# Kernel tuning notes

Hardware: AMD Instinct MI355X
Metric: run time of the kernel (lower is better)

## Reference

```python
import jax, jax.numpy as jnp
import numpy as np

V, D, NL, NH, HD, FF = 32000, 216, 11, 4, 54, 864
B, S = 2, 1024
EPS = 1e-5
THETA = 10000.0


def setup_inputs() -> dict:
    key = jax.random.key(0)
    ks = jax.random.split(key, 8)
    sc = 0.02
    return {
        "input_ids": jax.random.randint(ks[0], (B, S), 0, V),
        "embed": jax.random.normal(ks[1], (V, D), jnp.float32) * sc,
        "ln1_w": jnp.ones((NL, D), jnp.float32),
        "qkv_w": jax.random.normal(ks[2], (NL, 3 * D, D), jnp.float32) * sc,
        "o_w": jax.random.normal(ks[3], (NL, D, D), jnp.float32) * sc,
        "ln2_w": jnp.ones((NL, D), jnp.float32),
        "gate_w": jax.random.normal(ks[4], (NL, FF, D), jnp.float32) * sc,
        "up_w": jax.random.normal(ks[5], (NL, FF, D), jnp.float32) * sc,
        "down_w": jax.random.normal(ks[6], (NL, D, FF), jnp.float32) * sc,
        "norm_w": jnp.ones((D,), jnp.float32),
        "lm_head_w": jax.random.normal(ks[7], (V, D), jnp.float32) * sc,
    }


def _rmsnorm(x, w):
    return x * jax.lax.rsqrt(jnp.mean(x * x, axis=-1, keepdims=True) + EPS) * w


def _rope_tables(seq_len, dim, dtype):
    inv_freq = 1.0 / (THETA ** (jnp.arange(0, dim, 2, dtype=jnp.float32) / dim))
    t = jnp.arange(seq_len, dtype=jnp.float32)
    freqs = jnp.outer(t, inv_freq)              # [S, dim/2]
    emb = jnp.concatenate([freqs, freqs], -1)   # [S, dim]
    return jnp.cos(emb).astype(dtype), jnp.sin(emb).astype(dtype)


def _rotate_half(x):
    x1, x2 = x[..., : x.shape[-1] // 2], x[..., x.shape[-1] // 2:]
    return jnp.concatenate([-x2, x1], axis=-1)


def _forward(input_ids, embed, ln1_w, qkv_w, o_w, ln2_w, gate_w, up_w, down_w, norm_w, lm_head_w):
    b, s = input_ids.shape
    x = embed[input_ids]                                       # [B,S,D]
    cos, sin = _rope_tables(s, HD, x.dtype)                    # [S,HD]
    scale = HD ** -0.5
    neg_inf = jnp.finfo(x.dtype).min
    causal = jnp.triu(jnp.ones((s, s), bool), k=1)             # [S,S]

    for i in range(NL):
        # self-attention
        h = _rmsnorm(x, ln1_w[i])
        qkv = jnp.einsum("bsd,ed->bse", h, qkv_w[i])           # [B,S,3D]
        qkv = qkv.reshape(b, s, 3, NH, HD).transpose(2, 0, 3, 1, 4)  # [3,B,H,S,HD]
        q, k, v = qkv[0], qkv[1], qkv[2]
        q = q * cos + _rotate_half(q) * sin
        k = k * cos + _rotate_half(k) * sin
        scores = jnp.einsum("bhqd,bhkd->bhqk", q, k) * scale
        scores = jnp.where(causal, neg_inf, scores)
        attn = jax.nn.softmax(scores, axis=-1)
        out = jnp.einsum("bhqk,bhkd->bhqd", attn, v)
        out = out.transpose(0, 2, 1, 3).reshape(b, s, D)
        x = x + jnp.einsum("bsd,ed->bse", out, o_w[i])
        # SwiGLU MLP
        h = _rmsnorm(x, ln2_w[i])
        gate = jnp.einsum("bsd,fd->bsf", h, gate_w[i])
        up = jnp.einsum("bsd,fd->bsf", h, up_w[i])
        x = x + jnp.einsum("bsf,df->bsd", jax.nn.silu(gate) * up, down_w[i])

    x = _rmsnorm(x, norm_w)
    logits = jnp.einsum("bsd,vd->bsv", x, lm_head_w)           # [B,S,V]
    return logits


def reference(input_ids, embed, ln1_w, qkv_w, o_w, ln2_w, gate_w, up_w, down_w, norm_w, lm_head_w):
    return _forward(input_ids, embed, ln1_w, qkv_w, o_w, ln2_w, gate_w, up_w, down_w, norm_w, lm_head_w)
```

## Files before the change

### kernel.cpp

```cpp
#include <hip/hip_runtime.h>
#include <math.h>

#define Vv 32000
#define Dm 216
#define NLAY 11
#define NHh 4
#define HDd 54
#define FFf 864
#define Bb 2
#define Ss 1024
#define Tt (Bb*Ss)
#define EPSf 1e-5f
#define QKVW 648
#define KP 224
#define HDP 64
#define VTSZ (Ss*HDP)

typedef __attribute__((ext_vector_type(8))) short short8;
typedef __attribute__((ext_vector_type(8))) unsigned short ushort8;
typedef __attribute__((ext_vector_type(4))) float f32x4;

__device__ __forceinline__ unsigned short f2bf(float f) {
    unsigned int u = __float_as_uint(f);
    return (unsigned short)((u + 0x7fffu + ((u >> 16) & 1u)) >> 16);
}
__device__ __forceinline__ float bf2f(unsigned short u) {
    return __uint_as_float(((unsigned int)u) << 16);
}

__device__ void dev_convw(int relb, int nblk, const float* __restrict__ src,
                          unsigned short* __restrict__ dst,
                          int L, int N, int K, int Npad, int Kp, int rstride,
                          long dls, long doff) {
    size_t total = (size_t)L * Npad * Kp;
    for (size_t idx = (size_t)relb * 256 + threadIdx.x; idx < total;
         idx += (size_t)nblk * 256) {
        int k = (int)(idx % Kp);
        size_t rr = idx / Kp;
        int n = (int)(rr % Npad);
        int l = (int)(rr / Npad);
        float v = (n < N && k < K) ? src[((size_t)l * N + n) * K + k] : 0.f;
        dst[(size_t)l * dls + doff + (size_t)n * rstride + k] = f2bf(v);
    }
}

__device__ void dev_convqkv(int relb, int nblk, const float* __restrict__ src,
                            unsigned short* __restrict__ dst) {
    size_t total = (size_t)NLAY * 768 * KP;
    for (size_t idx = (size_t)relb * 256 + threadIdx.x; idx < total;
         idx += (size_t)nblk * 256) {
        int kk2 = (int)(idx % KP);
        size_t rr = idx / KP;
        int nr = (int)(rr % 768);
        int l = (int)(rr / 768);
        float v = 0.f;
        if (nr < 648 && kk2 < 216) {
            int srow;
            float sc = 1.f;
            if (nr < 432) {
                int which = nr >= 216;
                int cih = nr - which * 216;
                int head = cih / 54, dd = cih % 54;
                int j = dd >> 1, odd = dd & 1;
                srow = which * 216 + head * 54 + j + odd * 27;
                if (!which) sc = 0.13608276348795434f;
            } else srow = nr;
            v = src[((size_t)l * QKVW + srow) * 216 + kk2] * sc;
        }
        dst[idx] = f2bf(v);
    }
}

__device__ void dev_convowh(int relb, int nblk, const float* __restrict__ src,
                            unsigned short* __restrict__ dst) {
    size_t total = (size_t)NLAY * 4 * 224 * 64;
    for (size_t idx = (size_t)relb * 256 + threadIdx.x; idx < total;
         idx += (size_t)nblk * 256) {
        int kk = (int)(idx & 63);
        size_t rr = idx >> 6;
        int n = (int)(rr % 224);
        size_t rh = rr / 224;
        int h = (int)(rh & 3);
        int l = (int)(rh >> 2);
        float v = (n < 216 && kk < 54)
            ? src[((size_t)l * 216 + n) * 216 + h * 54 + kk] : 0.f;
        dst[idx] = f2bf(v);
    }
}

__global__ void k_setup(const int* __restrict__ ids, const float* __restrict__ emb,
                        float* __restrict__ x,
                        float* __restrict__ cost, float* __restrict__ sint,
                        unsigned int* __restrict__ zp, size_t zwords,
                        const float* __restrict__ qkv_w, unsigned short* __restrict__ qkvw,
                        const float* __restrict__ o_w, unsigned short* __restrict__ owh,
                        const float* __restrict__ gate_w, const float* __restrict__ up_w,
                        unsigned short* __restrict__ guw,
                        const float* __restrict__ down_w, unsigned short* __restrict__ dww,
                        const float* __restrict__ lm_w, unsigned short* __restrict__ lmw)
{
    const int b = blockIdx.x;
    const int tid = threadIdx.x;
    if (b < 2048) {
        int id = ids[b];
        for (int d = tid; d < Dm; d += 256)
            x[(size_t)b * Dm + d] = emb[(size_t)id * Dm + d];
    } else if (b < 2176) {
        for (int idx = (b - 2048) * 256 + tid; idx < 1024 * 27; idx += 128 * 256) {
            int s = idx / 27, j = idx % 27;
            float inv = powf(10000.0f, -2.0f * (float)j / 54.0f);
            float f = (float)s * inv;
            cost[s * 27 + j] = cosf(f);
            sint[s * 27 + j] = sinf(f);
        }
    } else if (b < 2432) {
        for (size_t i = (size_t)(b - 2176) * 256 + tid; i < zwords; i += (size_t)256 * 256)
            zp[i] = 0;
    } else if (b < 2944) {
        dev_convqkv(b - 2432, 512, qkv_w, qkvw);
    } else if (b < 3200) {
        dev_convowh(b - 2944, 256, o_w, owh);
    } else if (b < 3712) {
        dev_convw(b - 3200, 512, gate_w, guw, NLAY, FFf, Dm, 896, KP, 2 * KP, 1792L * KP, 0);
    } else if (b < 4224) {
        dev_convw(b - 3712, 512, up_w, guw, NLAY, FFf, Dm, 896, KP, 2 * KP, 1792L * KP, KP);
    } else if (b < 4736) {
        dev_convw(b - 4224, 512, down_w, dww, NLAY, Dm, FFf, 256, 864, 864, 256L * 864, 0);
    } else {
        dev_convw(b - 4736, 1024, lm_w, lmw, 1, Vv, Dm, Vv, KP, KP, (long)Vv * KP, 0);
    }
}

__device__ __forceinline__ void normpro(const float* __restrict__ x,
                                        const float* __restrict__ lnw, int m0,
                                        float* rsl, float* lnl, int tid) {
    __syncthreads();
    if (tid < 224) lnl[tid] = (tid < 216) ? lnw[tid] : 0.f;
    if (tid < 128) {
        int row = tid >> 1, half = tid & 1;
        const float* xr = x + (size_t)(m0 + row) * Dm + half * 108;
        float ss = 0.f;
        #pragma unroll
        for (int q = 0; q < 27; ++q) {
            float4 v = *(const float4*)(xr + q * 4);
            ss += v.x * v.x + v.y * v.y + v.z * v.z + v.w * v.w;
        }
        ss += __shfl_xor(ss, 1, 64);
        if (half == 0) rsl[row] = rsqrtf(ss / 216.f + EPSf);
    }
    __syncthreads();
}

__device__ __forceinline__ ushort8 normA(const float* __restrict__ x,
                                         const float* rsl, const float* lnl,
                                         int m0, int row, int base) {
    ushort8 o;
    if (base < 216) {
        const float* pp = x + (size_t)(m0 + row) * Dm + base;
        float r = rsl[row];
        float4 v0 = *(const float4*)pp;
        float4 v1 = *(const float4*)(pp + 4);
        o[0] = f2bf(v0.x * r * lnl[base + 0]);
        o[1] = f2bf(v0.y * r * lnl[base + 1]);
        o[2] = f2bf(v0.z * r * lnl[base + 2]);
        o[3] = f2bf(v0.w * r * lnl[base + 3]);
        o[4] = f2bf(v1.x * r * lnl[base + 4]);
        o[5] = f2bf(v1.y * r * lnl[base + 5]);
        o[6] = f2bf(v1.z * r * lnl[base + 6]);
        o[7] = f2bf(v1.w * r * lnl[base + 7]);
    } else {
        #pragma unroll
        for (int e = 0; e < 8; ++e) o[e] = 0;
    }
    return o;
}

__global__ __launch_bounds__(256) void k_qkv64(
    const float* __restrict__ x, const unsigned short* __restrict__ W,
    const float* __restrict__ lnw,
    const float* __restrict__ cost, const float* __restrict__ sint,
    unsigned short* __restrict__ Qb, unsigned short* __restrict__ Kb,
    unsigned short* __restrict__ Vt)
{
    __shared__ __align__(16) unsigned char SM[17664];
    unsigned short* lA = (unsigned short*)SM;
    unsigned short* lB = (unsigned short*)(SM + 8192);
    float* rsl = (float*)(SM + 16384);
    float* lnl = (float*)(SM + 16640);
    const int tid = threadIdx.x;
    const int m0 = blockIdx.x * 64;
    const int n0 = blockIdx.y * 64;
    normpro(x, lnw, m0, rsl, lnl, tid);

    const int wid = tid >> 6, lane = tid & 63;
    const int wr = wid >> 1, wc = wid & 1;
    const int r = tid >> 2, kc = tid & 3;
    const int lo = (r >> 4) * 512 + (((kc << 4) | (r & 15)) << 3);

    ushort8 ra = normA(x, rsl, lnl, m0, r, kc * 8);
    ushort8 rb = *(const ushort8*)(W + (size_t)(n0 + r) * KP + kc * 8);
    *(ushort8*)&lA[lo] = ra;
    *(ushort8*)&lB[lo] = rb;
    __syncthreads();

    f32x4 acc[2][2] = {};
    int cur = 0;
    for (int step = 0; step < 7; ++step) {
        const bool more = step < 6;
        if (more) {
            const int k0 = (step + 1) << 5;
            ra = normA(x, rsl, lnl, m0, r, k0 + kc * 8);
            rb = *(const ushort8*)(W + (size_t)(n0 + r) * KP + k0 + kc * 8);
        }
        short8 af[2], bf2[2];
        #pragma unroll
        for (int f = 0; f < 2; ++f) {
            af[f] = *(const short8*)&lA[cur * 2048 + (wr * 2 + f) * 512 + lane * 8];
            bf2[f] = *(const short8*)&lB[cur * 2048 + (wc * 2 + f) * 512 + lane * 8];
        }
        #pragma unroll
        for (int fm = 0; fm < 2; ++fm)
            #pragma unroll
            for (int fn = 0; fn < 2; ++fn)
                acc[fm][fn] = __builtin_amdgcn_mfma_f32_16x16x32_bf16(af[fm], bf2[fn], acc[fm][fn], 0, 0, 0);
        if (more) {
            const int nxt = cur ^ 1;
            *(ushort8*)&lA[nxt * 2048 + lo] = ra;
            *(ushort8*)&lB[nxt * 2048 + lo] = rb;
            __syncthreads();
            cur = nxt;
        }
    }

    const int lc16 = lane & 15, lg = lane >> 4;
    #pragma unroll
    for (int fm = 0; fm < 2; ++fm) {
        const int mrow = m0 + wr * 32 + fm * 16 + lg * 4;
        const int b = mrow >> 10;
        const int st0 = mrow & 1023;
        #pragma unroll
        for (int fn = 0; fn < 2; ++fn) {
            const int ncol = n0 + wc * 32 + fn * 16 + lc16;
            float v0 = acc[fm][fn][0], v1 = acc[fm][fn][1];
            float v2 = acc[fm][fn][2], v3 = acc[fm][fn][3];
            float p0 = __shfl_xor(v0, 1, 64);
            float p1 = __shfl_xor(v1, 1, 64);
            float p2 = __shfl_xor(v2, 1, 64);
            float p3 = __shfl_xor(v3, 1, 64);
            if (ncol < 432) {
                int which = ncol >= 216;
                int cih = ncol - which * 216;
                int head = cih / 54, dd = cih % 54;
                int j = dd >> 1;
                bool odd = dd & 1;
                unsigned short* dst = (which ? Kb : Qb) +
                    ((size_t)(b * NHh + head) * Ss + st0) * HDP + dd;
                float vv[4] = {v0, v1, v2, v3};
                float pp[4] = {p0, p1, p2, p3};
                #pragma unroll
                for (int i = 0; i < 4; ++i) {
                    float c = cost[(st0 + i) * 27 + j];
                    float sn = sint[(st0 + i) * 27 + j];
                    float o = odd ? (vv[i] * c + pp[i] * sn) : (vv[i] * c - pp[i] * sn);
                    dst[(size_t)i * HDP] = f2bf(o);
                }
            } else if (ncol < 648) {
                int d = ncol - 432;
                int head = d / 54, dd = d % 54;
                ushort4 pk;
                pk.x = f2bf(v0); pk.y = f2bf(v1); pk.z = f2bf(v2); pk.w = f2bf(v3);
                *(ushort4*)(Vt + (size_t)(b * NHh + head) * VTSZ + (size_t)dd * Ss + st0) = pk;
            }
        }
    }
}

__global__ __launch_bounds__(256) void k_gateup64(
    const float* __restrict__ x, const unsigned short* __restrict__ W,
    const float* __restrict__ lnw, unsigned short* __restrict__ act)
{
    __shared__ __align__(16) unsigned char SM[17664];
    unsigned short* lA = (unsigned short*)SM;
    unsigned short* lB = (unsigned short*)(SM + 8192);
    float* rsl = (float*)(SM + 16384);
    float* lnl = (float*)(SM + 16640);
    const int tid = threadIdx.x;
    const int m0 = blockIdx.x * 64;
    const int n0 = blockIdx.y * 64;
    normpro(x, lnw, m0, rsl, lnl, tid);

    const int wid = tid >> 6, lane = tid & 63;
    const int wr = wid >> 1, wc = wid & 1;
    const int r = tid >> 2, kc = tid & 3;
    const int lo = (r >> 4) * 512 + (((kc << 4) | (r & 15)) << 3);

    ushort8 ra = normA(x, rsl, lnl, m0, r, kc * 8);
    ushort8 rb = *(const ushort8*)(W + (size_t)(n0 + r) * KP + kc * 8);
    *(ushort8*)&lA[lo] = ra;
    *(ushort8*)&lB[lo] = rb;
    __syncthreads();

    f32x4 acc[2][2] = {};
    int cur = 0;
    for (int step = 0; step < 7; ++step) {
        const bool more = step < 6;
        if (more) {
            const int k0 = (step + 1) << 5;
            ra = normA(x, rsl, lnl, m0, r, k0 + kc * 8);
            rb = *(const ushort8*)(W + (size_t)(n0 + r) * KP + k0 + kc * 8);
        }
        short8 af[2], bf2[2];
        #pragma unroll
        for (int f = 0; f < 2; ++f) {
            af[f] = *(const short8*)&lA[cur * 2048 + (wr * 2 + f) * 512 + lane * 8];
            bf2[f] = *(const short8*)&lB[cur * 2048 + (wc * 2 + f) * 512 + lane * 8];
        }
        #pragma unroll
        for (int fm = 0; fm < 2; ++fm)
            #pragma unroll
            for (int fn = 0; fn < 2; ++fn)
                acc[fm][fn] = __builtin_amdgcn_mfma_f32_16x16x32_bf16(af[fm], bf2[fn], acc[fm][fn], 0, 0, 0);
        if (more) {
            const int nxt = cur ^ 1;
            *(ushort8*)&lA[nxt * 2048 + lo] = ra;
            *(ushort8*)&lB[nxt * 2048 + lo] = rb;
            __syncthreads();
            cur = nxt;
        }
    }

    const int lc16 = lane & 15, lg = lane >> 4;
    #pragma unroll
    for (int fm = 0; fm < 2; ++fm) {
        const int mrow = m0 + wr * 32 + fm * 16 + lg * 4;
        #pragma unroll
        for (int fn = 0; fn < 2; ++fn) {
            const int ncol = n0 + wc * 32 + fn * 16 + lc16;
            #pragma unroll
            for (int i = 0; i < 4; ++i) {
                float v = acc[fm][fn][i];
                float p = __shfl_xor(v, 1, 64);
                if ((lc16 & 1) == 0 && ncol < 1728) {
                    float y = v / (1.f + __expf(-v)) * p;
                    act[(size_t)(mrow + i) * 864 + (ncol >> 1)] = f2bf(y);
                }
            }
        }
    }
}

__global__ __launch_bounds__(256) void k_gemm_s(
    const unsigned short* __restrict__ A, const unsigned short* __restrict__ W,
    float* __restrict__ xio, int N, int Kp)
{
    __shared__ __align__(16) unsigned short lA[2][2048];
    __shared__ __align__(16) unsigned short lB[2][2048];
    const int tid = threadIdx.x;
    const int m0 = blockIdx.x * 64, n0 = blockIdx.y * 64;
    const int wid = tid >> 6, lane = tid & 63;
    const int wr = wid >> 1, wc = wid & 1;
    const int nsteps = Kp >> 5;
    const int r = tid >> 2, kc = tid & 3;
    const int lo = (r >> 4) * 512 + (((kc << 4) | (r & 15)) << 3);

    ushort8 ra = *(const ushort8*)(A + (size_t)(m0 + r) * Kp + kc * 8);
    ushort8 rb = *(const ushort8*)(W + (size_t)(n0 + r) * Kp + kc * 8);
    *(ushort8*)&lA[0][lo] = ra;
    *(ushort8*)&lB[0][lo] = rb;
    __syncthreads();

    f32x4 acc[2][2] = {};
    int cur = 0;
    for (int step = 0; step < nsteps; ++step) {
        const bool more = (step + 1) < nsteps;
        if (more) {
            const int k0 = (step + 1) << 5;
            ra = *(const ushort8*)(A + (size_t)(m0 + r) * Kp + k0 + kc * 8);
            rb = *(const ushort8*)(W + (size_t)(n0 + r) * Kp + k0 + kc * 8);
        }
        short8 af[2], bf2[2];
        #pragma unroll
        for (int f = 0; f < 2; ++f) {
            af[f] = *(const short8*)&lA[cur][(wr * 2 + f) * 512 + lane * 8];
            bf2[f] = *(const short8*)&lB[cur][(wc * 2 + f) * 512 + lane * 8];
        }
        #pragma unroll
        for (int fm = 0; fm < 2; ++fm)
            #pragma unroll
            for (int fn = 0; fn < 2; ++fn)
                acc[fm][fn] = __builtin_amdgcn_mfma_f32_16x16x32_bf16(af[fm], bf2[fn], acc[fm][fn], 0, 0, 0);
        if (more) {
            const int nxt = cur ^ 1;
            *(ushort8*)&lA[nxt][lo] = ra;
            *(ushort8*)&lB[nxt][lo] = rb;
            __syncthreads();
            cur = nxt;
        }
    }

    #pragma unroll
    for (int fm = 0; fm < 2; ++fm) {
        const int mrow = m0 + wr * 32 + fm * 16 + (lane >> 4) * 4;
        #pragma unroll
        for (int fn = 0; fn < 2; ++fn) {
            const int ncol = n0 + wc * 32 + fn * 16 + (lane & 15);
            if (ncol < N) {
                #pragma unroll
                for (int i = 0; i < 4; ++i) {
                    const size_t oi = (size_t)(mrow + i) * N + ncol;
                    xio[oi] += acc[fm][fn][i];
                }
            }
        }
    }
}

__global__ __launch_bounds__(256) void k_attn_o16(
    const unsigned short* __restrict__ Qb, const unsigned short* __restrict__ Kb,
    const unsigned short* __restrict__ Vt, const unsigned short* __restrict__ owh_l,
    float* __restrict__ x)
{
    __shared__ __align__(16) unsigned char SM[38912];
    const int tid = threadIdx.x;
    const int qu = blockIdx.x, h = blockIdx.y, b = blockIdx.z;
    const int bh = b * NHh + h;
    const int q0w = qu * 16;
    const int w = tid >> 6, lane = tid & 63;
    const int lc = lane & 15, lg = lane >> 4;

    unsigned short* Klw = (unsigned short*)(SM + w * 4096);
    unsigned short* Vlw = (unsigned short*)(SM + 16384 + w * 4096);
    unsigned short* Plw = (unsigned short*)(SM + 32768 + w * 1024);
    unsigned short* Ol  = (unsigned short*)(SM + 36864);

    const unsigned short* Qp = Qb + (size_t)bh * VTSZ;
    const unsigned short* Kpp = Kb + (size_t)bh * VTSZ;
    const unsigned short* Vp = Vt + (size_t)bh * VTSZ;
    const unsigned short* owh_h = owh_l + (size_t)h * 224 * 64;

    short8 qa[2];
    #pragma unroll
    for (int half = 0; half < 2; ++half)
        qa[half] = *(const short8*)(Qp + (size_t)(q0w + lc) * HDP + lg * 8 + half * 32);

    f32x4 o4[4] = {};
    float mreg[4] = {-3e38f, -3e38f, -3e38f, -3e38f};
    float lreg[4] = {0.f, 0.f, 0.f, 0.f};

    const int nt = (q0w + 15) / 32 + 1;
    for (int t = w; t < nt; t += 4) {
        const int kv0 = t * 32;
        for (int c = lane; c < 512; c += 64) {
            if (c < 256) {
                int sub = c >> 6;
                int kgrp = sub >> 1, dhalf = sub & 1;
                int dchunk = (c >> 4) & 3, krow = c & 15;
                *(ushort8*)&Klw[sub * 512 + (c & 63) * 8] =
                    *(const ushort8*)(Kpp + (size_t)(kv0 + kgrp * 16 + krow) * HDP + dhalf * 32 + dchunk * 8);
            } else {
                int c2 = c - 256;
                int dgrp = c2 >> 6;
                int kchunk = (c2 >> 4) & 3, dcol = c2 & 15;
                *(ushort8*)&Vlw[dgrp * 512 + (c2 & 63) * 8] =
                    *(const ushort8*)(Vp + (size_t)(dgrp * 16 + dcol) * Ss + kv0 + kchunk * 8);
            }
        }
        f32x4 s4[2] = {};
        #pragma unroll
        for (int dhalf = 0; dhalf < 2; ++dhalf) {
            #pragma unroll
            for (int kgrp = 0; kgrp < 2; ++kgrp) {
                short8 kf = *(const short8*)&Klw[(kgrp * 2 + dhalf) * 512 + lane * 8];
                s4[kgrp] = __builtin_amdgcn_mfma_f32_16x16x32_bf16(qa[dhalf], kf, s4[kgrp], 0, 0, 0);
            }
        }
        if (kv0 + 31 > q0w) {
            #pragma unroll
            for (int kgrp = 0; kgrp < 2; ++kgrp) {
                int kg = kv0 + kgrp * 16 + lc;
                #pragma unroll
                for (int rr = 0; rr < 4; ++rr) {
                    int qg = q0w + lg * 4 + rr;
                    if (kg > qg) s4[kgrp][rr] = -3e38f;
                }
            }
        }
        #pragma unroll
        for (int rr = 0; rr < 4; ++rr) {
            float rm = fmaxf(s4[0][rr], s4[1][rr]);
            #pragma unroll
            for (int msk = 1; msk < 16; msk <<= 1)
                rm = fmaxf(rm, __shfl_xor(rm, msk, 64));
            float mn = fmaxf(mreg[rr], rm);
            float esc = __expf(mreg[rr] - mn);
            mreg[rr] = mn;
            float e0 = __expf(s4[0][rr] - mn);
            float e1 = __expf(s4[1][rr] - mn);
            float rs = e0 + e1;
            #pragma unroll
            for (int msk = 1; msk < 16; msk <<= 1)
                rs += __shfl_xor(rs, msk, 64);
            lreg[rr] = lreg[rr] * esc + rs;
            #pragma unroll
            for (int db = 0; db < 4; ++db) o4[db][rr] *= esc;
            int q = lg * 4 + rr;
            Plw[(((lc >> 3)) * 16 + q) * 8 + (lc & 7)] = f2bf(e0);
            Plw[((2 + (lc >> 3)) * 16 + q) * 8 + (lc & 7)] = f2bf(e1);
        }
        short8 pa = *(const short8*)&Plw[(lg * 16 + lc) * 8];
        #pragma unroll
        for (int db = 0; db < 4; ++db) {
            short8 vf = *(const short8*)&Vlw[db * 512 + lane * 8];
            o4[db] = __builtin_amdgcn_mfma_f32_16x16x32_bf16(pa, vf, o4[db], 0, 0, 0);
        }
    }

    __syncthreads();
    float* mg = (float*)SM;
    const int slot = (w * 64 + lane) * 25;
    #pragma unroll
    for (int rr = 0; rr < 4; ++rr) { mg[slot + rr] = mreg[rr]; mg[slot + 4 + rr] = lreg[rr]; }
    #pragma unroll
    for (int db = 0; db < 4; ++db)
        #pragma unroll
        for (int rr = 0; rr < 4; ++rr) mg[slot + 8 + db * 4 + rr] = o4[db][rr];
    __syncthreads();
    if (w == 0) {
        #pragma unroll
        for (int rr = 0; rr < 4; ++rr) {
            float m = mreg[rr];
            #pragma unroll
            for (int ww = 1; ww < 4; ++ww)
                m = fmaxf(m, mg[(ww * 64 + lane) * 25 + rr]);
            float eself = __expf(mreg[rr] - m);
            float l = lreg[rr] * eself;
            float oc[4];
            #pragma unroll
            for (int db = 0; db < 4; ++db) oc[db] = o4[db][rr] * eself;
            #pragma unroll
            for (int ww = 1; ww < 4; ++ww) {
                int sl = (ww * 64 + lane) * 25;
                float e = __expf(mg[sl + rr] - m);
                l += mg[sl + 4 + rr] * e;
                #pragma unroll
                for (int db = 0; db < 4; ++db) oc[db] += mg[sl + 8 + db * 4 + rr] * e;
            }
            float inv = 1.f / l;
            int q = lg * 4 + rr;
            #pragma unroll
            for (int db = 0; db < 4; ++db) {
                int kchunk = db * 2 + (lc >> 3);
                Ol[(kchunk * 16 + q) * 8 + (lc & 7)] = f2bf(oc[db] * inv);
            }
        }
    }
    __syncthreads();

    f32x4 oacc[4] = {};
    #pragma unroll
    for (int ks = 0; ks < 2; ++ks) {
        short8 afr = *(const short8*)&Ol[ks * 512 + lane * 8];
        #pragma unroll
        for (int gi = 0; gi < 4; ++gi) {
            int g = gi * 4 + w;
            if (g < 14) {
                int n = g * 16 + lc;
                short8 bfr = *(const short8*)(owh_h + (size_t)n * 64 + ks * 32 + lg * 8);
                oacc[gi] = __builtin_amdgcn_mfma_f32_16x16x32_bf16(afr, bfr, oacc[gi], 0, 0, 0);
            }
        }
    }
    #pragma unroll
    for (int gi = 0; gi < 4; ++gi) {
        int g = gi * 4 + w;
        if (g < 14) {
            int col = g * 16 + lc;
            if (col < 216) {
                #pragma unroll
                for (int i = 0; i < 4; ++i) {
                    int row = b * Ss + q0w + lg * 4 + i;
                    atomicAdd(&x[(size_t)row * Dm + col], oacc[gi][i]);
                }
            }
        }
    }
}

template<int OUTM, bool NORMA>
__global__ __launch_bounds__(256, 2) void k_gemm_f(
    const void* __restrict__ Av, const unsigned short* __restrict__ W,
    const float* __restrict__ res, void* __restrict__ outv,
    const float* __restrict__ lnw, int N, int Kp)
{
    __shared__ __align__(16) unsigned short lds[2][2][4096];
    __shared__ float rsl[128];
    __shared__ float lnl[224];
    const int tid = threadIdx.x;
    const int m0 = blockIdx.x * 128;
    const int n0 = blockIdx.y * 128;
    const int wid = tid >> 6, lane = tid & 63;
    const int wr = wid >> 1, wc = wid & 1;
    const int nsteps = Kp >> 5;

    if constexpr (NORMA) {
        const float* Af = (const float*)Av;
        if (tid < 224) lnl[tid] = (tid < 216) ? lnw[tid] : 0.f;
        int row = tid >> 1, half = tid & 1;
        const float* xr = Af + (size_t)(m0 + row) * 216 + half * 108;
        float ss = 0.f;
        #pragma unroll
        for (int q = 0; q < 27; ++q) {
            float4 v = *(const float4*)(xr + q * 4);
            ss += v.x * v.x + v.y * v.y + v.z * v.z + v.w * v.w;
        }
        ss += __shfl_xor(ss, 1, 64);
        if (half == 0) rsl[row] = rsqrtf(ss / 216.f + EPSf);
        __syncthreads();
    }

    const int i0 = tid, i1 = tid + 256;
    const int rA0 = i0 >> 2, cA0 = i0 & 3;
    const int rA1 = i1 >> 2, cA1 = i1 & 3;
    const int lo0 = (rA0 >> 4) * 512 + (((cA0 << 4) | (rA0 & 15)) << 3);
    const int lo1 = (rA1 >> 4) * 512 + (((cA1 << 4) | (rA1 & 15)) << 3);

    auto loadA = [&](int row, int base) -> ushort8 {
        ushort8 o;
        if constexpr (NORMA) {
            if (base < 216) {
                const float* p = (const float*)Av + (size_t)(m0 + row) * 216 + base;
                float r = rsl[row];
                float4 v0 = *(const float4*)p;
                float4 v1 = *(const float4*)(p + 4);
                o[0] = f2bf(v0.x * r * lnl[base + 0]);
                o[1] = f2bf(v0.y * r * lnl[base + 1]);
                o[2] = f2bf(v0.z * r * lnl[base + 2]);
                o[3] = f2bf(v0.w * r * lnl[base + 3]);
                o[4] = f2bf(v1.x * r * lnl[base + 4]);
                o[5] = f2bf(v1.y * r * lnl[base + 5]);
                o[6] = f2bf(v1.z * r * lnl[base + 6]);
                o[7] = f2bf(v1.w * r * lnl[base + 7]);
            } else {
                #pragma unroll
                for (int e = 0; e < 8; ++e) o[e] = 0;
            }
        } else {
            o = *(const ushort8*)((const unsigned short*)Av + (size_t)(m0 + row) * Kp + base);
        }
        return o;
    };

    ushort8 ra0, ra1, rb0, rb1;
    ra0 = loadA(rA0, cA0 * 8);
    ra1 = loadA(rA1, cA1 * 8);
    rb0 = *(const ushort8*)(W + (size_t)(n0 + rA0) * Kp + cA0 * 8);
    rb1 = *(const ushort8*)(W + (size_t)(n0 + rA1) * Kp + cA1 * 8);
    *(ushort8*)&lds[0][0][lo0] = ra0;
    *(ushort8*)&lds[0][0][lo1] = ra1;
    *(ushort8*)&lds[0][1][lo0] = rb0;
    *(ushort8*)&lds[0][1][lo1] = rb1;
    __syncthreads();

    f32x4 acc[4][4] = {};
    int cur = 0;
    for (int step = 0; step < nsteps; ++step) {
        const bool more = (step + 1) < nsteps;
        if (more) {
            const int k0 = (step + 1) << 5;
            ra0 = loadA(rA0, k0 + cA0 * 8);
            ra1 = loadA(rA1, k0 + cA1 * 8);
            rb0 = *(const ushort8*)(W + (size_t)(n0 + rA0) * Kp + k0 + cA0 * 8);
            rb1 = *(const ushort8*)(W + (size_t)(n0 + rA1) * Kp + k0 + cA1 * 8);
        }
        short8 af[4], bf[4];
        #pragma unroll
        for (int f = 0; f < 4; ++f) {
            af[f] = *(const short8*)&lds[cur][0][(wr * 4 + f) * 512 + lane * 8];
            bf[f] = *(const short8*)&lds[cur][1][(wc * 4 + f) * 512 + lane * 8];
        }
        #pragma unroll
        for (int fm = 0; fm < 4; ++fm)
            #pragma unroll
            for (int fn = 0; fn < 4; ++fn)
                acc[fm][fn] = __builtin_amdgcn_mfma_f32_16x16x32_bf16(af[fm], bf[fn], acc[fm][fn], 0, 0, 0);
        if (more) {
            const int nxt = cur ^ 1;
            *(ushort8*)&lds[nxt][0][lo0] = ra0;
            *(ushort8*)&lds[nxt][0][lo1] = ra1;
            *(ushort8*)&lds[nxt][1][lo0] = rb0;
            *(ushort8*)&lds[nxt][1][lo1] = rb1;
            __syncthreads();
            cur = nxt;
        }
    }

    const int lc16 = lane & 15;
    #pragma unroll
    for (int fm = 0; fm < 4; ++fm) {
        const int mrow = m0 + wr * 64 + fm * 16 + (lane >> 4) * 4;
        #pragma unroll
        for (int fn = 0; fn < 4; ++fn) {
            const int ncol = n0 + wc * 64 + fn * 16 + lc16;
            if (ncol < N) {
                #pragma unroll
                for (int i = 0; i < 4; ++i) {
                    const size_t oi = (size_t)(mrow + i) * N + ncol;
                    float v = acc[fm][fn][i];
                    if (res) v += res[oi];
                    ((float*)outv)[oi] = v;
                }
            }
        }
    }
}

__global__ void k_embed(const int* __restrict__ ids, const float* __restrict__ emb,
                        float* __restrict__ x) {
    int t = blockIdx.x;
    int id = ids[t];
    for (int d = threadIdx.x; d < Dm; d += blockDim.x)
        x[(size_t)t * Dm + d] = emb[(size_t)id * Dm + d];
}

__global__ void k_rope_tables(float* __restrict__ cosb, float* __restrict__ sinb) {
    int s = blockIdx.x;
    for (int d = threadIdx.x; d < HDd; d += blockDim.x) {
        int j = d % (HDd / 2);
        float inv = powf(10000.0f, -2.0f * (float)j / (float)HDd);
        float f = (float)s * inv;
        cosb[s * HDd + d] = cosf(f);
        sinb[s * HDd + d] = sinf(f);
    }
}

__global__ void k_rmsnorm(const float* __restrict__ x, const float* __restrict__ w,
                          float* __restrict__ h) {
    int t = blockIdx.x;
    const float* xr = x + (size_t)t * Dm;
    float ss = 0.f;
    for (int d = threadIdx.x; d < Dm; d += 64) { float v = xr[d]; ss += v * v; }
    for (int o = 32; o; o >>= 1) ss += __shfl_down(ss, o, 64);
    float r = __shfl(ss, 0, 64);
    r = rsqrtf(r / (float)Dm + EPSf);
    for (int d = threadIdx.x; d < Dm; d += 64)
        h[(size_t)t * Dm + d] = xr[d] * r * w[d];
}

#define TS 16
__global__ void k_gemm(const float* __restrict__ A, const float* __restrict__ W,
                       const float* __restrict__ res, float* __restrict__ out,
                       int M, int N, int K) {
    __shared__ float As[TS][TS + 1];
    __shared__ float Wsm[TS][TS + 1];
    const int tx = threadIdx.x, ty = threadIdx.y;
    const int m = blockIdx.y * TS + ty;
    const int n = blockIdx.x * TS + tx;
    float acc = 0.f;
    for (int k0 = 0; k0 < K; k0 += TS) {
        int ka = k0 + tx;
        As[ty][tx] = (m < M && ka < K) ? A[(size_t)m * K + ka] : 0.f;
        int nw = blockIdx.x * TS + ty;
        Wsm[ty][tx] = (nw < N && ka < K) ? W[(size_t)nw * K + ka] : 0.f;
        __syncthreads();
        #pragma unroll
        for (int kk = 0; kk < TS; ++kk) acc += As[ty][kk] * Wsm[tx][kk];
        __syncthreads();
    }
    if (m < M && n < N) {
        float r = res ? res[(size_t)m * N + n] : 0.f;
        out[(size_t)m * N + n] = r + acc;
    }
}

__global__ void k_gateup(const float* __restrict__ A, const float* __restrict__ Wg,
                         const float* __restrict__ Wu, float* __restrict__ act,
                         int M, int N, int K) {
    __shared__ float As[TS][TS + 1];
    __shared__ float Gs[TS][TS + 1];
    __shared__ float Us[TS][TS + 1];
    const int tx = threadIdx.x, ty = threadIdx.y;
    const int m = blockIdx.y * TS + ty;
    const int n = blockIdx.x * TS + tx;
    float ag = 0.f, au = 0.f;
    for (int k0 = 0; k0 < K; k0 += TS) {
        int ka = k0 + tx;
        As[ty][tx] = (m < M && ka < K) ? A[(size_t)m * K + ka] : 0.f;
        int nw = blockIdx.x * TS + ty;
        Gs[ty][tx] = (nw < N && ka < K) ? Wg[(size_t)nw * K + ka] : 0.f;
        Us[ty][tx] = (nw < N && ka < K) ? Wu[(size_t)nw * K + ka] : 0.f;
        __syncthreads();
        #pragma unroll
        for (int kk = 0; kk < TS; ++kk) {
            ag += As[ty][kk] * Gs[tx][kk];
            au += As[ty][kk] * Us[tx][kk];
        }
        __syncthreads();
    }
    if (m < M && n < N) {
        float sg = ag / (1.f + expf(-ag));
        act[(size_t)m * N + n] = sg * au;
    }
}

__global__ void k_rope(float* __restrict__ qkv, const float* __restrict__ cosb,
                       const float* __restrict__ sinb) {
    const int t = blockIdx.x;
    const int s = t % Ss;
    float* base = qkv + (size_t)t * QKVW;
    const int HALF = HDd / 2;
    int i = threadIdx.x;
    if (i < 2 * NHh * HALF) {
        int which = i / (NHh * HALF);
        int rem = i % (NHh * HALF);
        int hh = rem / HALF;
        int d = rem % HALF;
        float* ptr = base + which * Dm + hh * HDd;
        float x1 = ptr[d], x2 = ptr[d + HALF];
        float c1 = cosb[s * HDd + d], s1 = sinb[s * HDd + d];
        float c2 = cosb[s * HDd + d + HALF], s2 = sinb[s * HDd + d + HALF];
        ptr[d]        = x1 * c1 - x2 * s1;
        ptr[d + HALF] = x2 * c2 + x1 * s2;
    }
}

__global__ void k_attn(const float* __restrict__ qkv, float* __restrict__ aout) {
    const int q = blockIdx.x, h = blockIdx.y, b = blockIdx.z;
    const int tid = threadIdx.x;
    __shared__ float p[Ss];
    __shared__ float qv[HDd];
    __shared__ float rmax[4], rsum[4];
    const size_t base = (size_t)b * Ss * QKVW;
    const float* qrow = qkv + base + (size_t)q * QKVW + h * HDd;
    if (tid < HDd) qv[tid] = qrow[tid];
    __syncthreads();
    const int nk = q + 1;
    const float scale = 0.13608276348795434f;
    float lmax = -3.0e38f;
    for (int k = tid; k < nk; k += 256) {
        const float* krow = qkv + base + (size_t)k * QKVW + Dm + h * HDd;
        float acc = 0.f;
        #pragma unroll
        for (int d = 0; d < HDd; ++d) acc += qv[d] * krow[d];
        acc *= scale;
        p[k] = acc;
        lmax = fmaxf(lmax, acc);
    }
    for (int o = 32; o; o >>= 1) lmax = fmaxf(lmax, __shfl_down(lmax, o, 64));
    if ((tid & 63) == 0) rmax[tid >> 6] = lmax;
    __syncthreads();
    const float m = fmaxf(fmaxf(rmax[0], rmax[1]), fmaxf(rmax[2], rmax[3]));
    float lsum = 0.f;
    for (int k = tid; k < nk; k += 256) {
        float e = expf(p[k] - m);
        p[k] = e;
        lsum += e;
    }
    for (int o = 32; o; o >>= 1) lsum += __shfl_down(lsum, o, 64);
    if ((tid & 63) == 0) rsum[tid >> 6] = lsum;
    __syncthreads();
    const float inv = 1.f / (rsum[0] + rsum[1] + rsum[2] + rsum[3]);
    for (int d = tid; d < HDd; d += 256) {
        const float* vcol = qkv + base + 2 * Dm + h * HDd + d;
        float acc = 0.f;
        for (int k = 0; k < nk; ++k) acc += p[k] * vcol[(size_t)k * QKVW];
        aout[(size_t)(b * Ss + q) * Dm + h * HDd + d] = acc * inv;
    }
}

extern "C" void kernel_launch(void* const* d_in, const int* in_sizes, int n_in,
                              void* d_out, int out_size, void* d_ws, size_t ws_size,
                              hipStream_t stream) {
    const int*   ids    = (const int*)d_in[0];
    const float* emb    = (const float*)d_in[1];
    const float* ln1_w  = (const float*)d_in[2];
    const float* qkv_w  = (const float*)d_in[3];
    const float* o_w    = (const float*)d_in[4];
    const float* ln2_w  = (const float*)d_in[5];
    const float* gate_w = (const float*)d_in[6];
    const float* up_w   = (const float*)d_in[7];
    const float* down_w = (const float*)d_in[8];
    const float* norm_w = (const float*)d_in[9];
    const float* lm_w   = (const float*)d_in[10];
    float* out = (float*)d_out;

    char* base = (char*)d_ws;
    size_t off = 0;
    auto carve = [&](size_t bytes) -> char* {
        char* p = base + off;
        off += (bytes + 255) & ~(size_t)255;
        return p;
    };

    float* x     = (float*)carve((size_t)Tt * Dm * 4);
    float* cos27 = (float*)carve((size_t)Ss * 27 * 4);
    float* sin27 = (float*)carve((size_t)Ss * 27 * 4);
    unsigned short* Qb   = (unsigned short*)carve((size_t)Bb * NHh * VTSZ * 2);
    unsigned short* Kb   = (unsigned short*)carve((size_t)Bb * NHh * VTSZ * 2);
    unsigned short* Vt   = (unsigned short*)carve((size_t)Bb * NHh * VTSZ * 2);
    char* zend = base + off;
    unsigned short* act  = (unsigned short*)carve((size_t)Tt * FFf * 2);
    unsigned short* qkvw = (unsigned short*)carve((size_t)NLAY * 768 * KP * 2);
    unsigned short* owh  = (unsigned short*)carve((size_t)NLAY * 4 * 224 * 64 * 2);
    unsigned short* guw  = (unsigned short*)carve((size_t)NLAY * 1792 * KP * 2);
    unsigned short* dww  = (unsigned short*)carve((size_t)NLAY * 256 * 864 * 2);
    unsigned short* lmw  = (unsigned short*)carve((size_t)Vv * KP * 2);
    size_t need = off;

    if (ws_size >= need) {
        size_t zwords = (size_t)(zend - (char*)Qb) / 4;
        k_setup<<<5760, 256, 0, stream>>>(ids, emb, x, cos27, sin27,
            (unsigned int*)Qb, zwords, qkv_w, qkvw, o_w, owh,
            gate_w, up_w, guw, down_w, dww, lm_w, lmw);

        for (int l = 0; l < NLAY; ++l) {
            k_qkv64<<<dim3(32, 12), 256, 0, stream>>>(
                x, qkvw + (size_t)l * 768 * KP, ln1_w + (size_t)l * Dm,
                cos27, sin27, Qb, Kb, Vt);
            k_attn_o16<<<dim3(64, NHh, Bb), 256, 0, stream>>>(
                Qb, Kb, Vt, owh + (size_t)l * 4 * 224 * 64, x);
            k_gateup64<<<dim3(32, 28), 256, 0, stream>>>(
                x, guw + (size_t)l * 1792 * KP, ln2_w + (size_t)l * Dm, act);
            k_gemm_s<<<dim3(32, 4), 256, 0, stream>>>(
                act, dww + (size_t)l * 256 * 864, x, Dm, 864);
        }
        k_gemm_f<0, true><<<dim3(16, 250), 256, 0, stream>>>(
            x, lmw, nullptr, out, norm_w, Vv, KP);
    } else {
        float* ws = (float*)d_ws;
        size_t o2 = 0;
        float* x2    = ws + o2; o2 += (size_t)Tt * Dm;
        float* h2    = ws + o2; o2 += (size_t)Tt * Dm;
        float* qkv2  = ws + o2; o2 += (size_t)Tt * QKVW;
        float* aout2 = ws + o2; o2 += (size_t)Tt * Dm;
        float* act2  = ws + o2; o2 += (size_t)Tt * FFf;
        float* cosb2 = ws + o2; o2 += (size_t)Ss * HDd;
        float* sinb2 = ws + o2; o2 += (size_t)Ss * HDd;

        k_embed<<<Tt, 256, 0, stream>>>(ids, emb, x2);
        k_rope_tables<<<Ss, 64, 0, stream>>>(cosb2, sinb2);
        dim3 blk(TS, TS);
        for (int l = 0; l < NLAY; ++l) {
            k_rmsnorm<<<Tt, 64, 0, stream>>>(x2, ln1_w + (size_t)l * Dm, h2);
            k_gemm<<<dim3((QKVW + TS - 1) / TS, (Tt + TS - 1) / TS), blk, 0, stream>>>(
                h2, qkv_w + (size_t)l * QKVW * Dm, nullptr, qkv2, Tt, QKVW, Dm);
            k_rope<<<Tt, 256, 0, stream>>>(qkv2, cosb2, sinb2);
            k_attn<<<dim3(Ss, NHh, Bb), 256, 0, stream>>>(qkv2, aout2);
            k_gemm<<<dim3((Dm + TS - 1) / TS, (Tt + TS - 1) / TS), blk, 0, stream>>>(
                aout2, o_w + (size_t)l * Dm * Dm, x2, x2, Tt, Dm, Dm);
            k_rmsnorm<<<Tt, 64, 0, stream>>>(x2, ln2_w + (size_t)l * Dm, h2);
            k_gateup<<<dim3((FFf + TS - 1) / TS, (Tt + TS - 1) / TS), blk, 0, stream>>>(
                h2, gate_w + (size_t)l * FFf * Dm, up_w + (size_t)l * FFf * Dm, act2, Tt, FFf, Dm);
            k_gemm<<<dim3((Dm + TS - 1) / TS, (Tt + TS - 1) / TS), blk, 0, stream>>>(
                act2, down_w + (size_t)l * Dm * FFf, x2, x2, Tt, Dm, FFf);
        }
        k_rmsnorm<<<Tt, 64, 0, stream>>>(x2, norm_w, h2);
        k_gemm<<<dim3((Vv + TS - 1) / TS, (Tt + TS - 1) / TS), blk, 0, stream>>>(
            h2, lm_w, nullptr, out, Tt, Vv, Dm);
    }
}
```

Baseline: 902.4 us.

## Fuse SwiGLU gate/up and down projection into one per-16-row FFN kernel

Replaces the separate gate/up GEMM and down-projection GEMM with a single kernel that normalizes 16 rows, computes the SwiGLU activation into shared memory, and immediately applies the down projection with a residual add. This removes the global activation buffer round-trip and one launch per layer. In exchange, only 128 blocks run and each streams the full weight matrices directly from global memory without shared-memory staging, which lowers parallelism and weight reuse.

```diff
diff --git a/kernel.cpp b/kernel.cpp
--- a/kernel.cpp
+++ b/kernel.cpp
@@ -275,140 +275,93 @@
     }
 }
 
-__global__ __launch_bounds__(256) void k_gateup64(
-    const float* __restrict__ x, const unsigned short* __restrict__ W,
-    const float* __restrict__ lnw, unsigned short* __restrict__ act)
+__global__ __launch_bounds__(256) void k_ffn16(
+    const float* __restrict__ x_in, float* __restrict__ x,
+    const unsigned short* __restrict__ guw_l, const unsigned short* __restrict__ dww_l,
+    const float* __restrict__ lnw)
 {
-    __shared__ __align__(16) unsigned char SM[17664];
-    unsigned short* lA = (unsigned short*)SM;
-    unsigned short* lB = (unsigned short*)(SM + 8192);
-    float* rsl = (float*)(SM + 16384);
-    float* lnl = (float*)(SM + 16640);
+    __shared__ __align__(16) unsigned char SM[35776];
+    unsigned short* Al  = (unsigned short*)SM;
+    unsigned short* Act = (unsigned short*)(SM + 7168);
+    float* rsl = (float*)(SM + 34816);
+    float* lnl = (float*)(SM + 34880);
     const int tid = threadIdx.x;
-    const int m0 = blockIdx.x * 64;
-    const int n0 = blockIdx.y * 64;
-    normpro(x, lnw, m0, rsl, lnl, tid);
-
-    const int wid = tid >> 6, lane = tid & 63;
-    const int wr = wid >> 1, wc = wid & 1;
-    const int r = tid >> 2, kc = tid & 3;
-    const int lo = (r >> 4) * 512 + (((kc << 4) | (r & 15)) << 3);
-
-    ushort8 ra = normA(x, rsl, lnl, m0, r, kc * 8);
-    ushort8 rb = *(const ushort8*)(W + (size_t)(n0 + r) * KP + kc * 8);
-    *(ushort8*)&lA[lo] = ra;
-    *(ushort8*)&lB[lo] = rb;
-    __syncthreads();
-
-    f32x4 acc[2][2] = {};
-    int cur = 0;
-    for (int step = 0; step < 7; ++step) {
-        const bool more = step < 6;
-        if (more) {
-            const int k0 = (step + 1) << 5;
-            ra = normA(x, rsl, lnl, m0, r, k0 + kc * 8);
-            rb = *(const ushort8*)(W + (size_t)(n0 + r) * KP + k0 + kc * 8);
-        }
-        short8 af[2], bf2[2];
-        #pragma unroll
-        for (int f = 0; f < 2; ++f) {
-            af[f] = *(const short8*)&lA[cur * 2048 + (wr * 2 + f) * 512 + lane * 8];
-            bf2[f] = *(const short8*)&lB[cur * 2048 + (wc * 2 + f) * 512 + lane * 8];
-        }
-        #pragma unroll
-        for (int fm = 0; fm < 2; ++fm)
-            #pragma unroll
-            for (int fn = 0; fn < 2; ++fn)
-                acc[fm][fn] = __builtin_amdgcn_mfma_f32_16x16x32_bf16(af[fm], bf2[fn], acc[fm][fn], 0, 0, 0);
-        if (more) {
-            const int nxt = cur ^ 1;
-            *(ushort8*)&lA[nxt * 2048 + lo] = ra;
-            *(ushort8*)&lB[nxt * 2048 + lo] = rb;
-            __syncthreads();
-            cur = nxt;
-        }
-    }
-
-    const int lc16 = lane & 15, lg = lane >> 4;
+    const int m0 = blockIdx.x * 16;
+    const int w = tid >> 6, lane = tid & 63;
+    const int lc = lane & 15, lg = lane >> 4;
+
+    if (tid < 224) lnl[tid] = (tid < 216) ? lnw[tid] : 0.f;
+    if (tid < 32) {
+        int row = tid >> 1, half = tid & 1;
+        const float* xr = x_in + (size_t)(m0 + row) * Dm + half * 108;
+        float ss = 0.f;
+        #pragma unroll
+        for (int q = 0; q < 27; ++q) {
+            float4 v = *(const float4*)(xr + q * 4);
+            ss += v.x * v.x + v.y * v.y + v.z * v.z + v.w * v.w;
+        }
+        ss += __shfl_xor(ss, 1, 64);
+        if (half == 0) rsl[row] = rsqrtf(ss / 216.f + EPSf);
+    }
+    __syncthreads();
+
+    {
+        int c = tid;
+        int row = c / 28, kc8 = c % 28;
+        *(ushort8*)&Al[(kc8 * 16 + row) * 8] = normA(x_in, rsl, lnl, m0, row, kc8 * 8);
+        int c2 = tid + 256;
+        if (c2 < 448) {
+            int row2 = c2 / 28, k2 = c2 % 28;
+            *(ushort8*)&Al[(k2 * 16 + row2) * 8] = normA(x_in, rsl, lnl, m0, row2, k2 * 8);
+        }
+    }
+    __syncthreads();
+
+    for (int g = 0; g < 27; ++g) {
+        const int ncol0 = w * 432 + g * 16;
+        f32x4 acc = {};
+        #pragma unroll
+        for (int ks = 0; ks < 7; ++ks) {
+            short8 afr = *(const short8*)&Al[((ks * 4 + lg) * 16 + lc) * 8];
+            short8 bfr = *(const short8*)(guw_l + (size_t)(ncol0 + lc) * KP + ks * 32 + lg * 8);
+            acc = __builtin_amdgcn_mfma_f32_16x16x32_bf16(afr, bfr, acc, 0, 0, 0);
+        }
+        #pragma unroll
+        for (int i = 0; i < 4; ++i) {
+            float v = acc[i];
+            float p = __shfl_xor(v, 1, 64);
+            if ((lc & 1) == 0) {
+                int c = (ncol0 + lc) >> 1;
+                int row = lg * 4 + i;
+                float y = v / (1.f + __expf(-v)) * p;
+                Act[((c >> 3) * 16 + row) * 8 + (c & 7)] = f2bf(y);
+            }
+        }
+    }
+    __syncthreads();
+
+    f32x4 oacc[4] = {};
+    for (int ks = 0; ks < 27; ++ks) {
+        short8 afr = *(const short8*)&Act[((ks * 4 + lg) * 16 + lc) * 8];
+        #pragma unroll
+        for (int gi = 0; gi < 4; ++gi) {
+            int g = gi * 4 + w;
+            if (g < 14) {
+                short8 bfr = *(const short8*)(dww_l + (size_t)(g * 16 + lc) * 864 + ks * 32 + lg * 8);
+                oacc[gi] = __builtin_amdgcn_mfma_f32_16x16x32_bf16(afr, bfr, oacc[gi], 0, 0, 0);
+            }
+        }
+    }
     #pragma unroll
-    for (int fm = 0; fm < 2; ++fm) {
-        const int mrow = m0 + wr * 32 + fm * 16 + lg * 4;
-        #pragma unroll
-        for (int fn = 0; fn < 2; ++fn) {
-            const int ncol = n0 + wc * 32 + fn * 16 + lc16;
-            #pragma unroll
-            for (int i = 0; i < 4; ++i) {
-                float v = acc[fm][fn][i];
-                float p = __shfl_xor(v, 1, 64);
-                if ((lc16 & 1) == 0 && ncol < 1728) {
-                    float y = v / (1.f + __expf(-v)) * p;
-                    act[(size_t)(mrow + i) * 864 + (ncol >> 1)] = f2bf(y);
-                }
-            }
-        }
-    }
-}
-
-__global__ __launch_bounds__(256) void k_gemm_s(
-    const unsigned short* __restrict__ A, const unsigned short* __restrict__ W,
-    float* __restrict__ xio, int N, int Kp)
-{
-    __shared__ __align__(16) unsigned short lA[2][2048];
-    __shared__ __align__(16) unsigned short lB[2][2048];
-    const int tid = threadIdx.x;
-    const int m0 = blockIdx.x * 64, n0 = blockIdx.y * 64;
-    const int wid = tid >> 6, lane = tid & 63;
-    const int wr = wid >> 1, wc = wid & 1;
-    const int nsteps = Kp >> 5;
-    const int r = tid >> 2, kc = tid & 3;
-    const int lo = (r >> 4) * 512 + (((kc << 4) | (r & 15)) << 3);
-
-    ushort8 ra = *(const ushort8*)(A + (size_t)(m0 + r) * Kp + kc * 8);
-    ushort8 rb = *(const ushort8*)(W + (size_t)(n0 + r) * Kp + kc * 8);
-    *(ushort8*)&lA[0][lo] = ra;
-    *(ushort8*)&lB[0][lo] = rb;
-    __syncthreads();
-
-    f32x4 acc[2][2] = {};
-    int cur = 0;
-    for (int step = 0; step < nsteps; ++step) {
-        const bool more = (step + 1) < nsteps;
-        if (more) {
-            const int k0 = (step + 1) << 5;
-            ra = *(const ushort8*)(A + (size_t)(m0 + r) * Kp + k0 + kc * 8);
-            rb = *(const ushort8*)(W + (size_t)(n0 + r) * Kp + k0 + kc * 8);
-        }
-        short8 af[2], bf2[2];
-        #pragma unroll
-        for (int f = 0; f < 2; ++f) {
-            af[f] = *(const short8*)&lA[cur][(wr * 2 + f) * 512 + lane * 8];
-            bf2[f] = *(const short8*)&lB[cur][(wc * 2 + f) * 512 + lane * 8];
-        }
-        #pragma unroll
-        for (int fm = 0; fm < 2; ++fm)
-            #pragma unroll
-            for (int fn = 0; fn < 2; ++fn)
-                acc[fm][fn] = __builtin_amdgcn_mfma_f32_16x16x32_bf16(af[fm], bf2[fn], acc[fm][fn], 0, 0, 0);
-        if (more) {
-            const int nxt = cur ^ 1;
-            *(ushort8*)&lA[nxt][lo] = ra;
-            *(ushort8*)&lB[nxt][lo] = rb;
-            __syncthreads();
-            cur = nxt;
-        }
-    }
-
-    #pragma unroll
-    for (int fm = 0; fm < 2; ++fm) {
-        const int mrow = m0 + wr * 32 + fm * 16 + (lane >> 4) * 4;
-        #pragma unroll
-        for (int fn = 0; fn < 2; ++fn) {
-            const int ncol = n0 + wc * 32 + fn * 16 + (lane & 15);
-            if (ncol < N) {
+    for (int gi = 0; gi < 4; ++gi) {
+        int g = gi * 4 + w;
+        if (g < 14) {
+            int col = g * 16 + lc;
+            if (col < 216) {
                 #pragma unroll
                 for (int i = 0; i < 4; ++i) {
-                    const size_t oi = (size_t)(mrow + i) * N + ncol;
-                    xio[oi] += acc[fm][fn][i];
+                    size_t oi = (size_t)(m0 + lg * 4 + i) * Dm + col;
+                    x[oi] += oacc[gi][i];
                 }
             }
         }
@@ -898,7 +851,6 @@
     unsigned short* Kb   = (unsigned short*)carve((size_t)Bb * NHh * VTSZ * 2);
     unsigned short* Vt   = (unsigned short*)carve((size_t)Bb * NHh * VTSZ * 2);
     char* zend = base + off;
-    unsigned short* act  = (unsigned short*)carve((size_t)Tt * FFf * 2);
     unsigned short* qkvw = (unsigned short*)carve((size_t)NLAY * 768 * KP * 2);
     unsigned short* owh  = (unsigned short*)carve((size_t)NLAY * 4 * 224 * 64 * 2);
     unsigned short* guw  = (unsigned short*)carve((size_t)NLAY * 1792 * KP * 2);
@@ -918,10 +870,9 @@
                 cos27, sin27, Qb, Kb, Vt);
             k_attn_o16<<<dim3(64, NHh, Bb), 256, 0, stream>>>(
                 Qb, Kb, Vt, owh + (size_t)l * 4 * 224 * 64, x);
-            k_gateup64<<<dim3(32, 28), 256, 0, stream>>>(
-                x, guw + (size_t)l * 1792 * KP, ln2_w + (size_t)l * Dm, act);
-            k_gemm_s<<<dim3(32, 4), 256, 0, stream>>>(
-                act, dww + (size_t)l * 256 * 864, x, Dm, 864);
+            k_ffn16<<<128, 256, 0, stream>>>(
+                x, x, guw + (size_t)l * 1792 * KP, dww + (size_t)l * 256 * 864,
+                ln2_w + (size_t)l * Dm);
         }
         k_gemm_f<0, true><<<dim3(16, 250), 256, 0, stream>>>(
             x, lmw, nullptr, out, norm_w, Vv, KP);
```

After: 1.458 ms. +61.6%, slower.
